# Kernel tuning notes

Measured on AMD Instinct MI355X. Metric: run time of the kernel, lower is better.

## Reference

```python
import jax, jax.numpy as jnp
import numpy as np

STRIDE = 8.0
NUM_CLASSES = 80
IGNORE_THR = 0.5
ANCHORS = np.array([[10.,13.],[16.,30.],[33.,23.]], dtype=np.float32)
TOTAL = np.array([[10.,13.],[16.,30.],[33.,23.],[30.,61.],[62.,45.],[59.,119.],[116.,90.],[156.,198.],[373.,326.]], dtype=np.float32)
# total-anchor index -> local anchor index (anchors_mask = [0,1,2] for this head), else -1
LUT = np.array([0,1,2,-1,-1,-1,-1,-1,-1], dtype=np.int32)


def _safe_log(p):
    # matches torch BCELoss log clamping at -100 (and avoids nan grads at p==0)
    return jnp.where(p > 0, jnp.log(jnp.where(p > 0, p, 1.0)), -100.0)


def _bce(p, t):
    return -(t * _safe_log(p) + (1.0 - t) * _safe_log(1.0 - p))


def _smooth_l1(p, t):
    d = jnp.abs(p - t)
    return jnp.where(d < 1.0, 0.5 * d * d, d - 0.5)


def _iou(b1, b2):
    # center-format (cx, cy, w, h) boxes, broadcastable on leading dims
    b1x1 = b1[..., 0] - b1[..., 2] * 0.5; b1x2 = b1[..., 0] + b1[..., 2] * 0.5
    b1y1 = b1[..., 1] - b1[..., 3] * 0.5; b1y2 = b1[..., 1] + b1[..., 3] * 0.5
    b2x1 = b2[..., 0] - b2[..., 2] * 0.5; b2x2 = b2[..., 0] + b2[..., 2] * 0.5
    b2y1 = b2[..., 1] - b2[..., 3] * 0.5; b2y2 = b2[..., 1] + b2[..., 3] * 0.5
    iw = jnp.clip(jnp.minimum(b1x2, b2x2) - jnp.maximum(b1x1, b2x1), 0.0)
    ih = jnp.clip(jnp.minimum(b1y2, b2y2) - jnp.maximum(b1y1, b2y1), 0.0)
    inter = iw * ih
    a1 = (b1x2 - b1x1) * (b1y2 - b1y1)
    a2 = (b2x2 - b2x1) * (b2y2 - b2y1)
    return inter / (a1 + a2 - inter + 1e-16)


def _forward(input, targets):
    bs, _, in_h, in_w = input.shape
    A, C = ANCHORS.shape[0], NUM_CLASSES
    sa = jnp.asarray(ANCHORS) / STRIDE   # [A,2] scaled anchors
    sta = jnp.asarray(TOTAL) / STRIDE    # [9,2] scaled total anchors
    pred = input.reshape(bs, A, 5 + C, in_h, in_w).transpose(0, 1, 3, 4, 2)  # [B,A,H,W,5+C]
    x = jax.nn.sigmoid(pred[..., 0]); y = jax.nn.sigmoid(pred[..., 1])
    w = pred[..., 2]; h = pred[..., 3]
    conf = jax.nn.sigmoid(pred[..., 4])
    pred_cls = jax.nn.sigmoid(pred[..., 5:])
    gxg = jnp.arange(in_w, dtype=input.dtype)
    gyg = jnp.arange(in_h, dtype=input.dtype)
    pb_x = x + gxg[None, None, None, :]
    pb_y = y + gyg[None, None, :, None]
    pb_w = jnp.exp(w) * sa[None, :, 0, None, None]
    pb_h = jnp.exp(h) * sa[None, :, 1, None, None]
    pred_boxes = jax.lax.stop_gradient(jnp.stack([pb_x, pb_y, pb_w, pb_h], -1))  # [B,A,H,W,4] (.data in torch)

    # ---- get_target, vectorized gather/compute/scatter ----
    T = targets.shape[1]
    valid = jnp.sum(targets, -1) != 0                                     # [B,T]
    gx = targets[..., 1] * in_w; gy = targets[..., 2] * in_h
    gw = targets[..., 3] * in_w; gh = targets[..., 4] * in_h
    gi = gx.astype(jnp.int32); gj = gy.astype(jnp.int32)                  # int() truncation (gx,gy >= 0)
    # anchor matching: IoU of (0,0,gw,gh) against (0,0,aw,ah) for the 9 total anchors
    gt0 = jnp.stack([jnp.zeros_like(gw), jnp.zeros_like(gw), gw, gh], -1)  # [B,T,4]
    an0 = jnp.concatenate([jnp.zeros_like(sta), sta], -1)                  # [9,4]
    a_iou = _iou(gt0[:, :, None, :], an0[None, None, :, :])                # [B,T,9]
    best_n = jnp.argmax(a_iou, -1)                                         # [B,T]
    ai = jnp.asarray(LUT)[best_n]                                          # local anchor index or -1
    write = valid & (ai >= 0)
    ai_w = jnp.where(write, ai, A)                                         # A is OOB -> dropped scatter
    aic = jnp.clip(ai, 0, A - 1)
    # ignore mask: IoU of each gt box against all predicted boxes of its image
    gt = jnp.stack([gx, gy, gw, gh], -1)                                   # [B,T,4]
    p_iou = _iou(gt[:, :, None, None, None, :], pred_boxes[:, None])       # [B,T,A,H,W]
    ignore = jnp.any((p_iou >= IGNORE_THR) & valid[:, :, None, None, None], axis=1)  # [B,A,H,W]
    b_idx = jnp.broadcast_to(jnp.arange(bs)[:, None], (bs, T))
    z = jnp.zeros((bs, A, in_h, in_w), input.dtype)
    def scat(vals):
        return z.at[b_idx, ai_w, gj, gi].set(vals.astype(input.dtype), mode='drop')
    mask = scat(jnp.ones_like(gx))
    scales = scat(2.0 - targets[..., 3] * targets[..., 4])
    tx = scat(gx - gi.astype(input.dtype))
    ty = scat(gy - gj.astype(input.dtype))
    tw = scat(jnp.log(gw / sa[aic, 0] + 1e-16))
    th = scat(jnp.log(gh / sa[aic, 1] + 1e-16))
    cls_idx = targets[..., 0].astype(jnp.int32)
    tcls = jnp.zeros((bs, A, in_h, in_w, C), input.dtype).at[b_idx, ai_w, gj, gi, cls_idx].set(1.0, mode='drop')
    noobj = jnp.minimum(1.0 - ignore.astype(input.dtype), 1.0 - mask)
    n_obj = jnp.sum(valid).astype(input.dtype)

    loss_x = jnp.sum(scales * _bce(x * mask, tx)) / n_obj
    loss_y = jnp.sum(scales * _bce(y * mask, ty)) / n_obj
    loss_w = jnp.sum(scales * _smooth_l1(w * mask, tw)) / n_obj
    loss_h = jnp.sum(scales * _smooth_l1(h * mask, th)) / n_obj
    loss_conf = jnp.sum(_bce(conf * mask, mask)) / n_obj + 0.5 * jnp.sum(_bce(conf * noobj, jnp.zeros_like(conf))) / n_obj
    # bce(pred_cls[mask==1], tcls[mask==1]).sum() == masked full sum (bce>=0, mask binary)
    loss_cls = jnp.sum(mask[..., None] * _bce(pred_cls, tcls)) / n_obj
    loss = 2.5 * (loss_x + loss_y) + 2.5 * (loss_w + loss_h) + 1.0 * loss_conf + 1.0 * loss_cls
    return jnp.stack([loss, loss_x, loss_y, loss_w, loss_h, loss_conf, loss_cls])


def setup_inputs():
    key = jax.random.key(0)
    k1, k2 = jax.random.split(key)
    inp = jax.random.normal(k1, (16, 255, 76, 76), dtype=jnp.float32)
    tgt = jax.random.uniform(k2, (16, 50, 5), dtype=jnp.float32)  # (cls, cx, cy, w, h) in (0,1)
    return {"input": inp, "targets": tgt}


def reference(input, targets):
    return _forward(input, targets)
```

## Files before the change

kernel.cpp:

```cpp
#include <hip/hip_runtime.h>
#include <cstddef>

#define NB 16
#define NT 50
#define NA 3
#define NH 76
#define NW 76
#define NC 80
#define HWSZ (NH*NW)
#define CPB 1024
#define NBLKX ((HWSZ + CPB - 1) / CPB)
#define NBLK (NBLKX * NB * NA)
#define NTARG (NB * NT)
#define WS_ACC  NBLK
#define WS_NOBJ (NBLK + 6)

__constant__ float d_taw[9] = {1.25f,2.0f,4.125f,3.75f,7.75f,7.375f,14.5f,19.5f,46.625f};
__constant__ float d_tah[9] = {1.625f,3.75f,2.875f,7.625f,5.625f,14.875f,11.25f,24.75f,40.75f};
__constant__ float d_saw[3] = {1.25f,2.0f,4.125f};
__constant__ float d_sah[3] = {1.625f,3.75f,2.875f};

__device__ __forceinline__ float safelog(float p) {
    return p > 0.f ? logf(p) : -100.f;
}
__device__ __forceinline__ float bce(float p, float t) {
    return -(t * safelog(p) + (1.f - t) * safelog(1.f - p));
}
__device__ __forceinline__ float sl1(float p, float t) {
    float d = fabsf(p - t);
    return d < 1.f ? 0.5f * d * d : d - 0.5f;
}
__device__ __forceinline__ float sigmoidf(float z) { return 1.f / (1.f + expf(-z)); }

struct TRec {
    bool valid, write;
    int ai, gi, gj, cls;
    float gx, gy, gw, gh;
};

__device__ __forceinline__ TRec decode(const float* __restrict__ tp) {
    TRec r;
    float t0 = tp[0], t1 = tp[1], t2 = tp[2], t3 = tp[3], t4 = tp[4];
    r.valid = (t0 + t1 + t2 + t3 + t4) != 0.f;
    r.gx = t1 * NW; r.gy = t2 * NH; r.gw = t3 * NW; r.gh = t4 * NH;
    r.gi = (int)r.gx; r.gj = (int)r.gy;
    float best = -1.f; int bn = 0;
    #pragma unroll
    for (int n = 0; n < 9; n++) {
        float inter = fminf(r.gw, d_taw[n]) * fminf(r.gh, d_tah[n]);
        float iou = inter / (r.gw * r.gh + d_taw[n] * d_tah[n] - inter + 1e-16f);
        if (iou > best) { best = iou; bn = n; }
    }
    r.ai = (bn < NA) ? bn : -1;
    r.write = r.valid && (r.ai >= 0);
    r.cls = (int)t0;
    return r;
}

__global__ __launch_bounds__(256) void k_main(const float* __restrict__ in,
                                              const float* __restrict__ tg,
                                              float* __restrict__ ws) {
    const int tid = threadIdx.x;
    const int wid = tid >> 6, lane = tid & 63;

    __shared__ __align__(16) float st[NT][8];
    __shared__ int s_nm, s_moff[NT];
    __shared__ float red[4];
    __shared__ int s_nmat, s_nobj;
    __shared__ int s_mt[NTARG];
    __shared__ float s_acc[6];

    if (blockIdx.y == NB * NA) {
        if (blockIdx.x != 0) return;
        if (tid == 0) { s_nmat = 0; s_nobj = 0; }
        if (tid < 6) s_acc[tid] = 0.f;
        __syncthreads();

        int cval = 0;
        #pragma unroll
        for (int rr = 0; rr < 4; rr++) {
            int idx = tid + rr * 256;
            if (idx < NTARG) {
                TRec tr = decode(tg + (size_t)idx * 5);
                if (tr.valid) cval++;
                if (tr.write) { int slot = atomicAdd(&s_nmat, 1); s_mt[slot] = idx; }
            }
        }
        #pragma unroll
        for (int off = 32; off > 0; off >>= 1) cval += __shfl_down(cval, off);
        if (lane == 0) atomicAdd(&s_nobj, cval);
        __syncthreads();

        const int nmat = s_nmat;
        for (int e = wid; e < nmat; e += 4) {
            const int t = s_mt[e];
            const int b = t / NT, tloc = t - b * NT;
            TRec r; r.valid = false; r.write = false;
            r.ai = -1; r.gi = -1; r.gj = -1; r.cls = 0;
            r.gx = r.gy = r.gw = r.gh = 0.f;
            float txl = 0.f, tyl = 0.f, twl = 0.f, thl = 0.f, scl = 0.f;
            if (lane < NT) {
                r = decode(tg + ((size_t)b * NT + lane) * 5);
                txl = r.gx - (float)r.gi; tyl = r.gy - (float)r.gj;
                int aic = r.ai < 0 ? 0 : r.ai;
                twl = logf(r.gw / d_saw[aic] + 1e-16f);
                thl = logf(r.gh / d_sah[aic] + 1e-16f);
                scl = 2.f - (r.gw / (float)NW) * (r.gh / (float)NH);
            }
            const int a  = __shfl(r.ai, tloc);
            const int gi = __shfl(r.gi, tloc);
            const int gj = __shfl(r.gj, tloc);
            bool match = r.write && (r.ai == a) && (r.gi == gi) && (r.gj == gj);
            unsigned long long mb = __ballot(match);
            int tlast = 63 - __clzll((long long)mb);
            if (tloc != tlast) continue;
            unsigned long long m0 = 0ull; unsigned m1 = 0u;
            unsigned long long mm = mb;
            while (mm) {
                int l = __ffsll(mm) - 1; mm &= mm - 1;
                int c = __shfl(r.cls, l);
                if (c < 64) m0 |= 1ull << c; else m1 |= 1u << (c - 64);
            }
            float tx = __shfl(txl, tlast), ty = __shfl(tyl, tlast);
            float tw = __shfl(twl, tlast), th = __shfl(thl, tlast);
            float sc = __shfl(scl, tlast);
            const size_t cb = ((size_t)b * 255 + (size_t)a * 85) * HWSZ
                            + (size_t)(gj * NW + gi);
            float z5 = (lane < 5) ? in[cb + (size_t)lane * HWSZ] : 0.f;
            float zx = __shfl(z5, 0), zy = __shfl(z5, 1), zww = __shfl(z5, 2),
                  zhh = __shfl(z5, 3), zcf = __shfl(z5, 4);
            float zca = in[cb + (size_t)(5 + lane) * HWSZ];
            float zcb = (lane < 16) ? in[cb + (size_t)(69 + lane) * HWSZ] : 0.f;
            float tca = ((m0 >> lane) & 1ull) ? 1.f : 0.f;
            float lcls = bce(sigmoidf(zca), tca);
            if (lane < 16) {
                float tcb = ((m1 >> lane) & 1u) ? 1.f : 0.f;
                lcls += bce(sigmoidf(zcb), tcb);
            }
            #pragma unroll
            for (int off = 32; off > 0; off >>= 1) lcls += __shfl_down(lcls, off);
            if (lane == 0) {
                atomicAdd(&s_acc[0], sc * bce(sigmoidf(zx), tx));
                atomicAdd(&s_acc[1], sc * bce(sigmoidf(zy), ty));
                atomicAdd(&s_acc[2], sc * sl1(zww, tw));
                atomicAdd(&s_acc[3], sc * sl1(zhh, th));
                atomicAdd(&s_acc[4], -safelog(sigmoidf(zcf)));
                atomicAdd(&s_acc[5], lcls);
            }
        }
        __syncthreads();
        if (tid < 6) ws[WS_ACC + tid] = s_acc[tid];
        if (tid == 6) ws[WS_NOBJ] = (float)s_nobj;
        return;
    }

    const int b = blockIdx.y / NA;
    const int a = blockIdx.y % NA;
    const int base = blockIdx.x * CPB;

    if (tid == 0) s_nm = 0;
    __syncthreads();
    if (tid < NT) {
        TRec r = decode(tg + ((size_t)b * NT + tid) * 5);
        float x1 = r.gx - r.gw * 0.5f, y1 = r.gy - r.gh * 0.5f;
        float x2 = r.gx + r.gw * 0.5f, y2 = r.gy + r.gh * 0.5f;
        float* o = st[tid];
        o[0] = x1; o[1] = y1; o[2] = x2; o[3] = y2;
        o[4] = r.valid ? (x2 - x1) * (y2 - y1) : __builtin_inff();
        if (r.write && r.ai == a) {
            int off = r.gj * NW + r.gi - base;
            if (off >= 0 && off < CPB) {
                int slot = atomicAdd(&s_nm, 1);
                s_moff[slot] = off;
            }
        }
    }
    __syncthreads();

    const float* ib = in + (size_t)(b * 255 + a * 85) * HWSZ;
    bool act[4]; int q[4];
    float zc[4], pxa[4], pxb[4], pya[4], pyb[4], pa[4];
    #pragma unroll
    for (int c = 0; c < 4; c++) {
        int p = base + c * 256 + tid;
        act[c] = p < HWSZ;
        q[c] = act[c] ? p : 0;
        float zx = ib[q[c]], zy = ib[HWSZ + q[c]], zw = ib[2 * HWSZ + q[c]],
              zh = ib[3 * HWSZ + q[c]];
        zc[c] = ib[4 * HWSZ + q[c]];
        int j = q[c] / NW, i = q[c] - j * NW;
        float x = sigmoidf(zx), y = sigmoidf(zy);
        float pbx = x + (float)i, pby = y + (float)j;
        float pbw = expf(zw) * d_saw[a], pbh = expf(zh) * d_sah[a];
        pxa[c] = pbx - pbw * 0.5f; pxb[c] = pbx + pbw * 0.5f;
        pya[c] = pby - pbh * 0.5f; pyb[c] = pby + pbh * 0.5f;
        pa[c] = (pxb[c] - pxa[c]) * (pyb[c] - pya[c]);
    }

    bool ig[4] = {false, false, false, false};
    for (int tb = 0; tb < NT; tb += 5) {
        float4 B[5]; float A_[5];
        #pragma unroll
        for (int u = 0; u < 5; u++) {
            B[u] = *(const float4*)&st[tb + u][0];
            A_[u] = st[tb + u][4];
        }
        #pragma unroll
        for (int u = 0; u < 5; u++) {
            #pragma unroll
            for (int c = 0; c < 4; c++) {
                float iw = fmaxf(fminf(B[u].z, pxb[c]) - fmaxf(B[u].x, pxa[c]), 0.f);
                float ih = fmaxf(fminf(B[u].w, pyb[c]) - fmaxf(B[u].y, pya[c]), 0.f);
                if (3.f * (iw * ih) >= A_[u] + pa[c]) ig[c] = true;
            }
        }
    }

    const int nm = s_nm;
    bool mm[4] = {false, false, false, false};
    for (int e = 0; e < nm; e++) {
        int mo = s_moff[e];
        #pragma unroll
        for (int c = 0; c < 4; c++) mm[c] |= (mo == c * 256 + tid);
    }
    float lc = 0.f;
    #pragma unroll
    for (int c = 0; c < 4; c++)
        if (act[c] && !mm[c] && !ig[c]) lc += 0.5f * (-safelog(1.f - sigmoidf(zc[c])));

    float s = lc;
    #pragma unroll
    for (int off = 32; off > 0; off >>= 1) s += __shfl_down(s, off);
    if (lane == 0) red[wid] = s;
    __syncthreads();
    if (tid == 0)
        ws[blockIdx.y * NBLKX + blockIdx.x] = red[0] + red[1] + red[2] + red[3];
}

__global__ __launch_bounds__(64) void k_final(const float* __restrict__ ws,
                                              float* __restrict__ out) {
    const int lane = threadIdx.x;
    float s = 0.f;
    for (int i = lane; i < NBLK; i += 64) s += ws[i];
    #pragma unroll
    for (int off = 32; off > 0; off >>= 1) s += __shfl_down(s, off);
    if (lane == 0) {
        float n = ws[WS_NOBJ];
        float lx = ws[WS_ACC + 0] / n, ly = ws[WS_ACC + 1] / n;
        float lw = ws[WS_ACC + 2] / n, lh = ws[WS_ACC + 3] / n;
        float lcf = (ws[WS_ACC + 4] + s) / n, lcl = ws[WS_ACC + 5] / n;
        out[0] = 2.5f * (lx + ly) + 2.5f * (lw + lh) + lcf + lcl;
        out[1] = lx; out[2] = ly; out[3] = lw; out[4] = lh; out[5] = lcf; out[6] = lcl;
    }
}

extern "C" void kernel_launch(void* const* d_in, const int* in_sizes, int n_in,
                              void* d_out, int out_size, void* d_ws, size_t ws_size,
                              hipStream_t stream) {
    const float* input   = (const float*)d_in[0];
    const float* targets = (const float*)d_in[1];
    float* out = (float*)d_out;
    float* ws  = (float*)d_ws;

    dim3 grid(NBLKX, NB * NA + 1);
    k_main<<<grid, 256, 0, stream>>>(input, targets, ws);
    k_final<<<1, 64, 0, stream>>>(ws, out);
}
```

Before: 145.8 us.

## Spread matched-target loss work across many blocks, one wavefront per target

The single serial block that handled every matched target, together with the atomic shared accumulators, is replaced by 200 extra blocks in a 1D grid. Each wavefront processes one target and writes its six partial losses to workspace. The valid-object count and the final reduction of all partials move into a wider k_final kernel. This removes the tail of one block looping over up to 800 targets, in exchange for more workspace traffic and a larger final reduction.

```diff
diff --git a/kernel.cpp b/kernel.cpp
--- a/kernel.cpp
+++ b/kernel.cpp
@@ -10,10 +10,10 @@
 #define HWSZ (NH*NW)
 #define CPB 1024
 #define NBLKX ((HWSZ + CPB - 1) / CPB)
-#define NBLK (NBLKX * NB * NA)
+#define NBULK (NBLKX * NB * NA)
 #define NTARG (NB * NT)
-#define WS_ACC  NBLK
-#define WS_NOBJ (NBLK + 6)
+#define NSPB  ((NTARG + 3) / 4)
+#define WS_T NBULK
 
 __constant__ float d_taw[9] = {1.25f,2.0f,4.125f,3.75f,7.75f,7.375f,14.5f,19.5f,46.625f};
 __constant__ float d_tah[9] = {1.625f,3.75f,2.875f,7.625f,5.625f,14.875f,11.25f,24.75f,40.75f};
@@ -62,101 +62,86 @@
                                               float* __restrict__ ws) {
     const int tid = threadIdx.x;
     const int wid = tid >> 6, lane = tid & 63;
-
-    __shared__ __align__(16) float st[NT][8];
-    __shared__ int s_nm, s_moff[NT];
-    __shared__ float red[4];
-    __shared__ int s_nmat, s_nobj;
-    __shared__ int s_mt[NTARG];
-    __shared__ float s_acc[6];
-
-    if (blockIdx.y == NB * NA) {
-        if (blockIdx.x != 0) return;
-        if (tid == 0) { s_nmat = 0; s_nobj = 0; }
-        if (tid < 6) s_acc[tid] = 0.f;
-        __syncthreads();
-
-        int cval = 0;
-        #pragma unroll
-        for (int rr = 0; rr < 4; rr++) {
-            int idx = tid + rr * 256;
-            if (idx < NTARG) {
-                TRec tr = decode(tg + (size_t)idx * 5);
-                if (tr.valid) cval++;
-                if (tr.write) { int slot = atomicAdd(&s_nmat, 1); s_mt[slot] = idx; }
-            }
-        }
-        #pragma unroll
-        for (int off = 32; off > 0; off >>= 1) cval += __shfl_down(cval, off);
-        if (lane == 0) atomicAdd(&s_nobj, cval);
-        __syncthreads();
-
-        const int nmat = s_nmat;
-        for (int e = wid; e < nmat; e += 4) {
-            const int t = s_mt[e];
-            const int b = t / NT, tloc = t - b * NT;
-            TRec r; r.valid = false; r.write = false;
-            r.ai = -1; r.gi = -1; r.gj = -1; r.cls = 0;
-            r.gx = r.gy = r.gw = r.gh = 0.f;
-            float txl = 0.f, tyl = 0.f, twl = 0.f, thl = 0.f, scl = 0.f;
-            if (lane < NT) {
-                r = decode(tg + ((size_t)b * NT + lane) * 5);
-                txl = r.gx - (float)r.gi; tyl = r.gy - (float)r.gj;
-                int aic = r.ai < 0 ? 0 : r.ai;
-                twl = logf(r.gw / d_saw[aic] + 1e-16f);
-                thl = logf(r.gh / d_sah[aic] + 1e-16f);
-                scl = 2.f - (r.gw / (float)NW) * (r.gh / (float)NH);
-            }
+    const int bid = blockIdx.x;
+
+    if (bid >= NBULK) {
+        const int t = (bid - NBULK) * 4 + wid;
+        const int b = t / NT, tloc = t - b * NT;
+
+        TRec r; r.valid = false; r.write = false;
+        r.ai = -1; r.gi = -1; r.gj = -1; r.cls = 0;
+        r.gx = r.gy = r.gw = r.gh = 0.f;
+        float txl = 0.f, tyl = 0.f, twl = 0.f, thl = 0.f, scl = 0.f;
+        if (lane < NT) {
+            r = decode(tg + ((size_t)b * NT + lane) * 5);
+            txl = r.gx - (float)r.gi; tyl = r.gy - (float)r.gj;
+            int aic = r.ai < 0 ? 0 : r.ai;
+            twl = logf(r.gw / d_saw[aic] + 1e-16f);
+            thl = logf(r.gh / d_sah[aic] + 1e-16f);
+            scl = 2.f - (r.gw / (float)NW) * (r.gh / (float)NH);
+        }
+        const int wflag = __shfl((int)r.write, tloc);
+        float v0 = 0.f, v1 = 0.f, v2 = 0.f, v3 = 0.f, v4 = 0.f, v5 = 0.f;
+        if (wflag) {
             const int a  = __shfl(r.ai, tloc);
             const int gi = __shfl(r.gi, tloc);
             const int gj = __shfl(r.gj, tloc);
             bool match = r.write && (r.ai == a) && (r.gi == gi) && (r.gj == gj);
             unsigned long long mb = __ballot(match);
             int tlast = 63 - __clzll((long long)mb);
-            if (tloc != tlast) continue;
-            unsigned long long m0 = 0ull; unsigned m1 = 0u;
-            unsigned long long mm = mb;
-            while (mm) {
-                int l = __ffsll(mm) - 1; mm &= mm - 1;
-                int c = __shfl(r.cls, l);
-                if (c < 64) m0 |= 1ull << c; else m1 |= 1u << (c - 64);
+            if (tloc == tlast) {
+                unsigned long long m0 = 0ull; unsigned m1 = 0u;
+                unsigned long long mm = mb;
+                while (mm) {
+                    int l = __ffsll(mm) - 1; mm &= mm - 1;
+                    int c = __shfl(r.cls, l);
+                    if (c < 64) m0 |= 1ull << c; else m1 |= 1u << (c - 64);
+                }
+                float tx = __shfl(txl, tlast), ty = __shfl(tyl, tlast);
+                float tw = __shfl(twl, tlast), th = __shfl(thl, tlast);
+                float sc = __shfl(scl, tlast);
+                const size_t cb = ((size_t)b * 255 + (size_t)a * 85) * HWSZ
+                                + (size_t)(gj * NW + gi);
+                float z5 = (lane < 5) ? in[cb + (size_t)lane * HWSZ] : 0.f;
+                float zx = __shfl(z5, 0), zy = __shfl(z5, 1), zww = __shfl(z5, 2),
+                      zhh = __shfl(z5, 3), zcf = __shfl(z5, 4);
+                float zca = in[cb + (size_t)(5 + lane) * HWSZ];
+                float zcb = (lane < 16) ? in[cb + (size_t)(69 + lane) * HWSZ] : 0.f;
+                float tca = ((m0 >> lane) & 1ull) ? 1.f : 0.f;
+                float lcls = bce(sigmoidf(zca), tca);
+                if (lane < 16) {
+                    float tcb = ((m1 >> lane) & 1u) ? 1.f : 0.f;
+                    lcls += bce(sigmoidf(zcb), tcb);
+                }
+                #pragma unroll
+                for (int off = 32; off > 0; off >>= 1) lcls += __shfl_down(lcls, off);
+                if (lane == 0) {
+                    v0 = sc * bce(sigmoidf(zx), tx);
+                    v1 = sc * bce(sigmoidf(zy), ty);
+                    v2 = sc * sl1(zww, tw);
+                    v3 = sc * sl1(zhh, th);
+                    v4 = -safelog(sigmoidf(zcf));
+                    v5 = lcls;
+                }
             }
-            float tx = __shfl(txl, tlast), ty = __shfl(tyl, tlast);
-            float tw = __shfl(twl, tlast), th = __shfl(thl, tlast);
-            float sc = __shfl(scl, tlast);
-            const size_t cb = ((size_t)b * 255 + (size_t)a * 85) * HWSZ
-                            + (size_t)(gj * NW + gi);
-            float z5 = (lane < 5) ? in[cb + (size_t)lane * HWSZ] : 0.f;
-            float zx = __shfl(z5, 0), zy = __shfl(z5, 1), zww = __shfl(z5, 2),
-                  zhh = __shfl(z5, 3), zcf = __shfl(z5, 4);
-            float zca = in[cb + (size_t)(5 + lane) * HWSZ];
-            float zcb = (lane < 16) ? in[cb + (size_t)(69 + lane) * HWSZ] : 0.f;
-            float tca = ((m0 >> lane) & 1ull) ? 1.f : 0.f;
-            float lcls = bce(sigmoidf(zca), tca);
-            if (lane < 16) {
-                float tcb = ((m1 >> lane) & 1u) ? 1.f : 0.f;
-                lcls += bce(sigmoidf(zcb), tcb);
-            }
-            #pragma unroll
-            for (int off = 32; off > 0; off >>= 1) lcls += __shfl_down(lcls, off);
-            if (lane == 0) {
-                atomicAdd(&s_acc[0], sc * bce(sigmoidf(zx), tx));
-                atomicAdd(&s_acc[1], sc * bce(sigmoidf(zy), ty));
-                atomicAdd(&s_acc[2], sc * sl1(zww, tw));
-                atomicAdd(&s_acc[3], sc * sl1(zhh, th));
-                atomicAdd(&s_acc[4], -safelog(sigmoidf(zcf)));
-                atomicAdd(&s_acc[5], lcls);
-            }
-        }
-        __syncthreads();
-        if (tid < 6) ws[WS_ACC + tid] = s_acc[tid];
-        if (tid == 6) ws[WS_NOBJ] = (float)s_nobj;
+        }
+        if (lane == 0) {
+            float* wt = ws + WS_T + t;
+            wt[0 * NTARG] = v0; wt[1 * NTARG] = v1; wt[2 * NTARG] = v2;
+            wt[3 * NTARG] = v3; wt[4 * NTARG] = v4; wt[5 * NTARG] = v5;
+        }
         return;
     }
 
-    const int b = blockIdx.y / NA;
-    const int a = blockIdx.y % NA;
-    const int base = blockIdx.x * CPB;
+    const int bx = bid % NBLKX;
+    const int by = bid / NBLKX;
+    const int b = by / NA;
+    const int a = by % NA;
+    const int base = bx * CPB;
+
+    __shared__ __align__(16) float st[NT][8];
+    __shared__ int s_nm, s_moff[NT];
+    __shared__ float red[4];
 
     if (tid == 0) s_nm = 0;
     __syncthreads();
@@ -234,21 +219,47 @@
     if (lane == 0) red[wid] = s;
     __syncthreads();
     if (tid == 0)
-        ws[blockIdx.y * NBLKX + blockIdx.x] = red[0] + red[1] + red[2] + red[3];
-}
-
-__global__ __launch_bounds__(64) void k_final(const float* __restrict__ ws,
-                                              float* __restrict__ out) {
-    const int lane = threadIdx.x;
-    float s = 0.f;
-    for (int i = lane; i < NBLK; i += 64) s += ws[i];
-    #pragma unroll
-    for (int off = 32; off > 0; off >>= 1) s += __shfl_down(s, off);
+        ws[bid] = red[0] + red[1] + red[2] + red[3];
+}
+
+__global__ __launch_bounds__(256) void k_final(const float* __restrict__ ws,
+                                               const float* __restrict__ tg,
+                                               float* __restrict__ out) {
+    const int tid = threadIdx.x;
+    const int wid = tid >> 6, lane = tid & 63;
+    float acc[8] = {0.f, 0.f, 0.f, 0.f, 0.f, 0.f, 0.f, 0.f};
+
+    for (int t = tid; t < NTARG; t += 256) {
+        #pragma unroll
+        for (int k = 0; k < 6; k++) acc[k] += ws[WS_T + k * NTARG + t];
+    }
+    for (int i = tid; i < NBULK; i += 256) acc[6] += ws[i];
+    for (int t = tid; t < NTARG; t += 256) {
+        const float* tp = tg + (size_t)t * 5;
+        float s5 = tp[0] + tp[1] + tp[2] + tp[3] + tp[4];
+        if (s5 != 0.f) acc[7] += 1.f;
+    }
+
+    #pragma unroll
+    for (int k = 0; k < 8; k++) {
+        #pragma unroll
+        for (int off = 32; off > 0; off >>= 1) acc[k] += __shfl_down(acc[k], off);
+    }
+    __shared__ float red[4][8];
     if (lane == 0) {
-        float n = ws[WS_NOBJ];
-        float lx = ws[WS_ACC + 0] / n, ly = ws[WS_ACC + 1] / n;
-        float lw = ws[WS_ACC + 2] / n, lh = ws[WS_ACC + 3] / n;
-        float lcf = (ws[WS_ACC + 4] + s) / n, lcl = ws[WS_ACC + 5] / n;
+        #pragma unroll
+        for (int k = 0; k < 8; k++) red[wid][k] = acc[k];
+    }
+    __syncthreads();
+    if (tid == 0) {
+        float s[8];
+        #pragma unroll
+        for (int k = 0; k < 8; k++)
+            s[k] = red[0][k] + red[1][k] + red[2][k] + red[3][k];
+        float n = s[7];
+        float lx = s[0] / n, ly = s[1] / n;
+        float lw = s[2] / n, lh = s[3] / n;
+        float lcf = (s[4] + s[6]) / n, lcl = s[5] / n;
         out[0] = 2.5f * (lx + ly) + 2.5f * (lw + lh) + lcf + lcl;
         out[1] = lx; out[2] = ly; out[3] = lw; out[4] = lh; out[5] = lcf; out[6] = lcl;
     }
@@ -262,7 +273,6 @@
     float* out = (float*)d_out;
     float* ws  = (float*)d_ws;
 
-    dim3 grid(NBLKX, NB * NA + 1);
-    k_main<<<grid, 256, 0, stream>>>(input, targets, ws);
-    k_final<<<1, 64, 0, stream>>>(ws, out);
-}
+    k_main<<<dim3(NBULK + NSPB), 256, 0, stream>>>(input, targets, ws);
+    k_final<<<1, 256, 0, stream>>>(ws, targets, out);
+}
```

Measured after the change: 135.5 us. 7.0% less time.
